# Performance work log

Measured on AMD Instinct MI355X. Metric: run time of the kernel, lower is better.

## Reference

```python
import jax, jax.numpy as jnp
import numpy as np

B, M, E, K, V, O = 2048, 131072, 256, 128, 256, 256
TOP_K = 3
THRESH = 0.0  # retrieval_threshold; default 0.5 but lowered so memory path is exercised
EPS = 1e-8


def setup_inputs() -> dict:
    key = jax.random.key(0)
    ks = jax.random.split(key, 20)
    w = lambda k, shape: jax.random.normal(k, shape, jnp.float32) * 0.02
    return {
        'state_embedding': jax.random.normal(ks[0], (B, E), jnp.float32),
        'keys': jax.random.normal(ks[1], (M, K), jnp.float32),
        'values': jax.random.normal(ks[2], (M, V), jnp.float32),
        'k_w1': w(ks[3], (E, 512)), 'k_b1': jnp.zeros((512,), jnp.float32),
        'k_w2': w(ks[4], (512, K)), 'k_b2': jnp.zeros((K,), jnp.float32),
        'a_w1': w(ks[5], (E + V, 128)), 'a_b1': jnp.zeros((128,), jnp.float32),
        'a_w2': w(ks[6], (128, 1)), 'a_b2': jnp.zeros((1,), jnp.float32),
        'i_w1': w(ks[7], (E + V, 512)), 'i_b1': jnp.zeros((512,), jnp.float32),
        'i_w2': w(ks[8], (512, O)), 'i_b2': jnp.zeros((O,), jnp.float32),
        'f_w1': w(ks[9], (E, 512)), 'f_b1': jnp.zeros((512,), jnp.float32),
        'f_w2': w(ks[10], (512, O)), 'f_b2': jnp.zeros((O,), jnp.float32),
    }


def _mann_forward(state_embedding, keys, values,
                  k_w1, k_b1, k_w2, k_b2,
                  a_w1, a_b1, a_w2, a_b2,
                  i_w1, i_b1, i_w2, i_b2,
                  f_w1, f_b1, f_w2, f_b2):
    # key_encoder: Linear -> ReLU -> Linear   [B, K]
    query = jax.nn.relu(state_embedding @ k_w1 + k_b1) @ k_w2 + k_b2
    # cosine similarity between query and the whole key bank  [B, M]
    qn = query / jnp.maximum(jnp.linalg.norm(query, axis=-1, keepdims=True), EPS)
    kn = keys / jnp.maximum(jnp.linalg.norm(keys, axis=-1, keepdims=True), EPS)
    sims = qn @ kn.T
    # iterative argmax+mask with threshold break == top-k then threshold mask
    top_vals, top_idx = jax.lax.top_k(sims, TOP_K)          # [B, TOP_K]
    hit = top_vals >= THRESH                                 # [B, TOP_K]
    retrieved = values[top_idx]                              # [B, TOP_K, V] gather
    # attention over retrieved memories conditioned on the state
    state_rep = jnp.broadcast_to(state_embedding[:, None, :], (state_embedding.shape[0], TOP_K, E))
    attn_in = jnp.concatenate([state_rep, retrieved], axis=-1)  # [B, TOP_K, E+V]
    h = jnp.tanh(attn_in @ a_w1 + a_b1)
    logits = (h @ a_w2 + a_b2)[..., 0]                       # [B, TOP_K]
    logits = jnp.where(hit, logits, -1e9)
    attn = jax.nn.softmax(logits, axis=-1)                   # [B, TOP_K]
    mem_vec = jnp.einsum('bk,bkv->bv', attn, retrieved)      # [B, V]
    # integration path (memory hit) vs fallback projection (miss)
    combined = jnp.concatenate([state_embedding, mem_vec], axis=-1)
    integrated = jax.nn.relu(combined @ i_w1 + i_b1) @ i_w2 + i_b2
    fallback = jax.nn.relu(state_embedding @ f_w1 + f_b1) @ f_w2 + f_b2
    any_hit = jnp.any(hit, axis=-1, keepdims=True)
    return jnp.where(any_hit, integrated, fallback)          # [B, O]


def reference(state_embedding, keys, values,
              k_w1, k_b1, k_w2, k_b2,
              a_w1, a_b1, a_w2, a_b2,
              i_w1, i_b1, i_w2, i_b2,
              f_w1, f_b1, f_w2, f_b2):
    return _mann_forward(state_embedding, keys, values,
                         k_w1, k_b1, k_w2, k_b2,
                         a_w1, a_b1, a_w2, a_b2,
                         i_w1, i_b1, i_w2, i_b2,
                         f_w1, f_b1, f_w2, f_b2)
```

## Files before the change

### kernel.cpp

```cpp
#include <hip/hip_runtime.h>
#include <math.h>

#define B_SZ 2048
#define M_SZ 131072
#define E_SZ 256
#define K_SZ 128
#define V_SZ 256
#define O_SZ 256

#define NCH  32
#define CH   (M_SZ / NCH)
#define BT   128
#define STG  64
#define NSTG (CH / STG)

#define WS_QN    0
#define WS_QNB   (WS_QN + B_SZ * K_SZ)
#define WS_KNB   (WS_QNB + B_SZ * K_SZ / 2)
#define WS_RNK   (WS_KNB + M_SZ * K_SZ / 2)
#define WS_CAND  (WS_RNK + M_SZ)
#define WS_TVAL  (WS_CAND + B_SZ * NCH * 16 * 3)
#define WS_TIDX  (WS_TVAL + B_SZ * 3)
#define WS_HENC  WS_CAND
#define WS_MEM   WS_CAND
#define WS_H2    (WS_CAND + B_SZ * V_SZ)
#define WS_HIT   (WS_H2 + B_SZ * 512)

#define NEG_INF (-3.0e38f)

typedef __attribute__((ext_vector_type(8))) short short8;
typedef __attribute__((ext_vector_type(4))) float f32x4;

static __device__ __forceinline__ void gl_lds16(const void* gptr, void* ldsptr) {
  __builtin_amdgcn_global_load_lds(
      (const __attribute__((address_space(1))) unsigned int*)gptr,
      (__attribute__((address_space(3))) unsigned int*)ldsptr, 16, 0, 0);
}

static __device__ __forceinline__ unsigned short f2bf(float x) {
  unsigned u = __float_as_uint(x);
  unsigned r = (u + 0x7FFFu + ((u >> 16) & 1u)) >> 16;
  return (unsigned short)r;
}
static __device__ __forceinline__ unsigned flipbf(unsigned short h) {
  return (h & 0x8000u) ? (unsigned)(h ^ 0xFFFFu) : (unsigned)(h | 0x8000u);
}

static __device__ __forceinline__ void ins3m(float (&tv)[3], float v, int kidx) {
  float vm = __uint_as_float((__float_as_uint(v) & 0xFFFFF000u) | (unsigned)kidx);
  float m0 = fmaxf(tv[0], vm), c0 = fminf(tv[0], vm);
  float m1 = fmaxf(tv[1], c0), c1 = fminf(tv[1], c0);
  float m2 = fmaxf(tv[2], c1);
  tv[0] = m0; tv[1] = m1; tv[2] = m2;
}
static __device__ __forceinline__ void ins3e(float (&tv)[3], float vm) {
  float m0 = fmaxf(tv[0], vm), c0 = fminf(tv[0], vm);
  float m1 = fmaxf(tv[1], c0), c1 = fminf(tv[1], c0);
  float m2 = fmaxf(tv[2], c1);
  tv[0] = m0; tv[1] = m1; tv[2] = m2;
}

static __device__ __forceinline__ void ins3u(unsigned (&tv)[3], int (&ti)[3], unsigned v, int m) {
  if (v > tv[2]) {
    if (v > tv[1]) {
      if (v > tv[0]) {
        tv[2] = tv[1]; ti[2] = ti[1]; tv[1] = tv[0]; ti[1] = ti[0]; tv[0] = v; ti[0] = m;
      } else {
        tv[2] = tv[1]; ti[2] = ti[1]; tv[1] = v; ti[1] = m;
      }
    } else {
      tv[2] = v; ti[2] = m;
    }
  }
}

__global__ __launch_bounds__(256)
void mann_enc1(const float* __restrict__ state,
               const float* __restrict__ k_w1,
               const float* __restrict__ k_b1,
               float* __restrict__ henc) {
  const int t = threadIdx.x;
  const int c = blockIdx.y * 256 + t;
  const int b0 = blockIdx.x * 4;
  float acc[4];
  const float bias = k_b1[c];
#pragma unroll
  for (int r = 0; r < 4; ++r) acc[r] = bias;
#pragma unroll 8
  for (int k = 0; k < 256; ++k) {
    const float w = k_w1[k * 512 + c];
#pragma unroll
    for (int r = 0; r < 4; ++r)
      acc[r] += state[(size_t)(b0 + r) * E_SZ + k] * w;
  }
#pragma unroll
  for (int r = 0; r < 4; ++r)
    henc[(size_t)(b0 + r) * 512 + c] = fmaxf(acc[r], 0.f);
}

__global__ __launch_bounds__(256)
void mann_enc2(const float* __restrict__ henc,
               const float* __restrict__ k_w2,
               const float* __restrict__ k_b2,
               float* __restrict__ qn,
               unsigned short* __restrict__ qnb) {
  __shared__ float s_red[4][128];
  __shared__ float s_part[2][4];
  const int t = threadIdx.x;
  const int col = t & 127, half = t >> 7;
  const int b0 = blockIdx.x * 4;
  float acc[4];
  const float bias = (half == 0) ? k_b2[col] : 0.f;
#pragma unroll
  for (int r = 0; r < 4; ++r) acc[r] = bias;
  const int kb = half * 256;
#pragma unroll 8
  for (int k = 0; k < 256; ++k) {
    const float wv = k_w2[(kb + k) * 128 + col];
#pragma unroll
    for (int r = 0; r < 4; ++r)
      acc[r] += henc[(size_t)(b0 + r) * 512 + kb + k] * wv;
  }
  if (half == 1)
#pragma unroll
    for (int r = 0; r < 4; ++r) s_red[r][col] = acc[r];
  __syncthreads();
  if (half == 0) {
#pragma unroll
    for (int r = 0; r < 4; ++r) acc[r] += s_red[r][col];
    const int l = t & 63, w = t >> 6;
    float ss[4];
#pragma unroll
    for (int r = 0; r < 4; ++r) ss[r] = acc[r] * acc[r];
#pragma unroll
    for (int off = 32; off > 0; off >>= 1)
#pragma unroll
      for (int r = 0; r < 4; ++r) ss[r] += __shfl_down(ss[r], off);
    if (l == 0)
#pragma unroll
      for (int r = 0; r < 4; ++r) s_part[w][r] = ss[r];
  }
  __syncthreads();
  if (half == 0) {
#pragma unroll
    for (int r = 0; r < 4; ++r) {
      float rn = 1.0f / fmaxf(sqrtf(s_part[0][r] + s_part[1][r]), 1e-8f);
      float q = acc[r] * rn;
      qn[(size_t)(b0 + r) * K_SZ + t] = q;
      qnb[(size_t)(b0 + r) * K_SZ + t] = f2bf(q);
    }
  }
}

__global__ void mann_keyprep(const float* __restrict__ keys,
                             unsigned short* __restrict__ knbsw,
                             float* __restrict__ rnk) {
  const int lane = threadIdx.x & 63;
  const int row = blockIdx.x * 4 + (threadIdx.x >> 6);
  const float* kr = keys + (size_t)row * K_SZ;
  float a = kr[lane], c = kr[lane + 64];
  float s = a * a + c * c;
#pragma unroll
  for (int off = 32; off > 0; off >>= 1) s += __shfl_down(s, off);
  float rn = 1.0f / fmaxf(sqrtf(__shfl(s, 0)), 1e-8f);
  if (lane == 0) rnk[row] = rn;
  const int r7 = row & 7;
  const int lp = lane & 31;
  const int src = ((((lp) >> 2) ^ r7) << 3) | ((2 * lp) & 7);
  float a0 = __shfl(a, src), a1 = __shfl(a, src + 1);
  float c0 = __shfl(c, src), c1 = __shfl(c, src + 1);
  float x0 = (lane < 32) ? a0 : c0;
  float x1 = (lane < 32) ? a1 : c1;
  unsigned pack = ((unsigned)f2bf(x1 * rn) << 16) | (unsigned)f2bf(x0 * rn);
  ((unsigned*)(knbsw + (size_t)row * 128))[lane] = pack;
}

__global__ __launch_bounds__(512, 4)
void mann_sims_mfma(const unsigned short* __restrict__ qnb,
                    const unsigned short* __restrict__ knbsw,
                    unsigned* __restrict__ cand) {
  __shared__ unsigned short s_k[2 * STG * 128];
  const int t = threadIdx.x;
  const int w = t >> 6, l = t & 63;
  const int wk = w >> 2;
  const int wr = w & 3;
  const int lo = l & 15, g = l >> 4;
  const int chunk = blockIdx.x, bt = blockIdx.y;
  const int b0 = bt * BT + wr * 32;
  const int k0 = chunk * CH;

  short8 afrag[2][4];
#pragma unroll
  for (int rti = 0; rti < 2; ++rti)
#pragma unroll
    for (int ks = 0; ks < 4; ++ks)
      afrag[rti][ks] = *(const short8*)(qnb + (size_t)(b0 + rti * 16 + lo) * K_SZ + ks * 32 + g * 8);

  float tv[2][4][3];
#pragma unroll
  for (int a = 0; a < 2; ++a)
#pragma unroll
    for (int b = 0; b < 4; ++b)
#pragma unroll
      for (int c = 0; c < 3; ++c) tv[a][b][c] = NEG_INF;

  const int ev = lo * 256 + ((g ^ (lo & 7)) << 4);
  const int od = ev ^ 64;
  const char* pev = (const char*)s_k + ev + wk * 8192;
  const char* pod = (const char*)s_k + od + wk * 8192;

  const char* gbase = (const char*)knbsw + (size_t)k0 * 256;
  char* lds0 = (char*)s_k;

#define ISSUE_STAGE(S, BUF)                                                  \
  do {                                                                       \
    const char* g0 = gbase + (size_t)(S) * 16384;                            \
    char* l0 = lds0 + (BUF) * 16384;                                         \
    _Pragma("unroll")                                                        \
    for (int i = 0; i < 2; ++i) {                                            \
      int seg = i * 8 + w;                                                   \
      gl_lds16(g0 + seg * 1024 + l * 16, l0 + seg * 1024);                   \
    }                                                                        \
  } while (0)

#define STAGE_CORE(S, BUF)                                                   \
  do {                                                                       \
    f32x4 cbuf[2][2];                                                        \
    __builtin_amdgcn_s_setprio(1);                                           \
    _Pragma("unroll")                                                        \
    for (int ktl = 0; ktl < 2; ++ktl) {                                      \
      short8 b0v = *(const short8*)(pev + (BUF) * 16384 + ktl * 4096);       \
      short8 b1v = *(const short8*)(pod + (BUF) * 16384 + ktl * 4096);       \
      short8 b2v = *(const short8*)(pev + (BUF) * 16384 + ktl * 4096 + 128); \
      short8 b3v = *(const short8*)(pod + (BUF) * 16384 + ktl * 4096 + 128); \
      _Pragma("unroll")                                                      \
      for (int rti = 0; rti < 2; ++rti) {                                    \
        f32x4 acc = {0.f, 0.f, 0.f, 0.f};                                    \
        acc = __builtin_amdgcn_mfma_f32_16x16x32_bf16(afrag[rti][0], b0v, acc, 0, 0, 0); \
        acc = __builtin_amdgcn_mfma_f32_16x16x32_bf16(afrag[rti][1], b1v, acc, 0, 0, 0); \
        acc = __builtin_amdgcn_mfma_f32_16x16x32_bf16(afrag[rti][2], b2v, acc, 0, 0, 0); \
        acc = __builtin_amdgcn_mfma_f32_16x16x32_bf16(afrag[rti][3], b3v, acc, 0, 0, 0); \
        cbuf[rti][ktl] = acc;                                                \
      }                                                                      \
    }                                                                        \
    __builtin_amdgcn_s_setprio(0);                                           \
    _Pragma("unroll")                                                        \
    for (int ktl = 0; ktl < 2; ++ktl) {                                      \
      const int kidx = (S) * STG + (wk * 2 + ktl) * 16 + lo;                 \
      _Pragma("unroll")                                                      \
      for (int rti = 0; rti < 2; ++rti) {                                    \
        ins3m(tv[rti][0], cbuf[rti][ktl][0], kidx);                          \
        ins3m(tv[rti][1], cbuf[rti][ktl][1], kidx);                          \
        ins3m(tv[rti][2], cbuf[rti][ktl][2], kidx);                          \
        ins3m(tv[rti][3], cbuf[rti][ktl][3], kidx);                          \
      }                                                                      \
    }                                                                        \
  } while (0)

  ISSUE_STAGE(0, 0);

  for (int s = 0; s < NSTG; s += 2) {
    __syncthreads();
    if (s + 1 < NSTG) ISSUE_STAGE(s + 1, 1);
    STAGE_CORE(s, 0);
    __syncthreads();
    if (s + 2 < NSTG) ISSUE_STAGE(s + 2, 0);
    STAGE_CORE(s + 1, 1);
  }
#undef STAGE_CORE
#undef ISSUE_STAGE

  __syncthreads();
  unsigned* lm = (unsigned*)s_k;
  if (wk == 1) {
#pragma unroll
    for (int rti = 0; rti < 2; ++rti)
#pragma unroll
      for (int j = 0; j < 4; ++j)
#pragma unroll
        for (int slot = 0; slot < 3; ++slot)
          lm[((wr * 64 + l) * 2 + rti) * 12 + j * 3 + slot] =
              __float_as_uint(tv[rti][j][slot]);
  }
  __syncthreads();
  if (wk == 0) {
#pragma unroll
    for (int rti = 0; rti < 2; ++rti)
#pragma unroll
      for (int j = 0; j < 4; ++j)
#pragma unroll
        for (int slot = 0; slot < 3; ++slot) {
          float bv = __uint_as_float(lm[((wr * 64 + l) * 2 + rti) * 12 + j * 3 + slot]);
          ins3e(tv[rti][j], bv);
        }
#pragma unroll
    for (int rti = 0; rti < 2; ++rti) {
#pragma unroll
      for (int j = 0; j < 4; ++j) {
        int b = b0 + rti * 16 + g * 4 + j;
        size_t base = (((size_t)b * NCH + chunk) * 16 + lo) * 3;
#pragma unroll
        for (int slot = 0; slot < 3; ++slot) {
          unsigned bits = __float_as_uint(tv[rti][j][slot]);
          float val = __uint_as_float(bits & 0xFFFFF000u);
          unsigned idx = bits & 0xFFFu;
          unsigned p = (flipbf(f2bf(val)) << 16) | idx;
          cand[base + slot] = p;
        }
      }
    }
  }
}

__global__ void mann_merge_rescore(const unsigned* __restrict__ cand,
                                   const float* __restrict__ qn,
                                   const float* __restrict__ keys,
                                   const float* __restrict__ rnk,
                                   float* __restrict__ tval,
                                   int* __restrict__ tidx) {
  __shared__ unsigned s_pv[4][192];
  __shared__ int s_gi[4][192];
  __shared__ float s_ex[4][8];
  const int t = threadIdx.x;
  const int w = t >> 6, l = t & 63;
  const int b = blockIdx.x * 4 + w;
  const int NCAND = NCH * 16 * 3;

  unsigned pv[3] = {0u, 0u, 0u};
  int gi[3] = {0, 0, 0};
  for (int k = 0; k < NCAND / 64; ++k) {
    int i = l + k * 64;
    unsigned p = cand[(size_t)b * NCAND + i];
    int gidx = (i / 48) * CH + (int)(p & 0xFFFu);
    ins3u(pv, gi, p, gidx);
  }
#pragma unroll
  for (int j = 0; j < 3; ++j) { s_pv[w][l * 3 + j] = pv[j]; s_gi[w][l * 3 + j] = gi[j]; }
  __syncthreads();

  if (l == 0) {
    unsigned bv[8]; int bg[8];
#pragma unroll
    for (int j = 0; j < 8; ++j) { bv[j] = 0u; bg[j] = 0; }
    for (int i = 0; i < 192; ++i) {
      unsigned p = s_pv[w][i];
      if (p > bv[7]) {
        int gg = s_gi[w][i];
        int j = 7;
        while (j > 0 && p > bv[j - 1]) { bv[j] = bv[j - 1]; bg[j] = bg[j - 1]; --j; }
        bv[j] = p; bg[j] = gg;
      }
    }
#pragma unroll
    for (int j = 0; j < 8; ++j) s_gi[w][j] = bg[j];
  }
  __syncthreads();

  float q0 = qn[(size_t)b * K_SZ + l];
  float q1 = qn[(size_t)b * K_SZ + 64 + l];
#pragma unroll
  for (int d = 0; d < 8; ++d) {
    int idx = s_gi[w][d];
    float p = q0 * keys[(size_t)idx * K_SZ + l] + q1 * keys[(size_t)idx * K_SZ + 64 + l];
#pragma unroll
    for (int off = 32; off > 0; off >>= 1) p += __shfl_down(p, off);
    if (l == 0) s_ex[w][d] = p * rnk[idx];
  }
  __syncthreads();

  if (l == 0) {
    unsigned used = 0;
#pragma unroll
    for (int r = 0; r < 3; ++r) {
      float best = NEG_INF; int bd = 0;
      for (int d = 0; d < 8; ++d)
        if (!(used & (1u << d)) && s_ex[w][d] > best) { best = s_ex[w][d]; bd = d; }
      used |= (1u << bd);
      tval[b * 3 + r] = best;
      tidx[b * 3 + r] = s_gi[w][bd];
    }
  }
}

__global__ __launch_bounds__(128)
void mann_t1(const float* __restrict__ state,
             const float* __restrict__ values,
             const float* __restrict__ tval,
             const int* __restrict__ tidx,
             const float* __restrict__ a_w1, const float* __restrict__ a_b1,
             const float* __restrict__ a_w2, const float* __restrict__ a_b2,
             float* __restrict__ mem, int* __restrict__ hit) {
  __shared__ float s_h1[6][128];
  __shared__ float s_logit[6];
  __shared__ float s_attn[2][3];
  const int t = threadIdx.x;
  const int b0 = blockIdx.x * 2;

  float racc[2];
  {
    const float bias = a_b1[t];
#pragma unroll
    for (int r = 0; r < 2; ++r) racc[r] = bias;
  }
#pragma unroll 4
  for (int k = 0; k < 256; ++k) {
    const float w = a_w1[k * 128 + t];
#pragma unroll
    for (int r = 0; r < 2; ++r)
      racc[r] += state[(size_t)(b0 + r) * E_SZ + k] * w;
  }
  float pacc[6];
#pragma unroll
  for (int p = 0; p < 6; ++p) pacc[p] = racc[p / 3];
#pragma unroll 4
  for (int k = 0; k < 256; ++k) {
    const float w = a_w1[(256 + k) * 128 + t];
#pragma unroll
    for (int p = 0; p < 6; ++p) {
      const int vrow = tidx[(b0 + p / 3) * 3 + (p % 3)];
      pacc[p] += values[(size_t)vrow * V_SZ + k] * w;
    }
  }
#pragma unroll
  for (int p = 0; p < 6; ++p) s_h1[p][t] = tanhf(pacc[p]);
  __syncthreads();

  if (t < 48) {
    const int p = t >> 3, l8 = t & 7;
    float acc = 0.f;
    for (int i = l8; i < 128; i += 8)
      acc += s_h1[p][i] * a_w2[i];
#pragma unroll
    for (int off = 4; off > 0; off >>= 1) acc += __shfl_down(acc, off, 8);
    if (l8 == 0) s_logit[p] = acc + a_b2[0];
  }
  __syncthreads();

  if (t < 2) {
    const int b = b0 + t;
    bool h0 = tval[b * 3 + 0] >= 0.0f;
    bool h1 = tval[b * 3 + 1] >= 0.0f;
    bool h2 = tval[b * 3 + 2] >= 0.0f;
    float l0 = h0 ? s_logit[t * 3 + 0] : -1e9f;
    float l1 = h1 ? s_logit[t * 3 + 1] : -1e9f;
    float l2 = h2 ? s_logit[t * 3 + 2] : -1e9f;
    float mx = fmaxf(l0, fmaxf(l1, l2));
    float e0 = expf(l0 - mx), e1 = expf(l1 - mx), e2 = expf(l2 - mx);
    float inv = 1.0f / (e0 + e1 + e2);
    s_attn[t][0] = e0 * inv; s_attn[t][1] = e1 * inv; s_attn[t][2] = e2 * inv;
    hit[b] = (h0 || h1 || h2) ? 1 : 0;
  }
  __syncthreads();

#pragma unroll
  for (int r = 0; r < 2; ++r) {
    const int i0 = tidx[(b0 + r) * 3 + 0];
    const int i1 = tidx[(b0 + r) * 3 + 1];
    const int i2 = tidx[(b0 + r) * 3 + 2];
    const float a0 = s_attn[r][0], a1 = s_attn[r][1], a2 = s_attn[r][2];
#pragma unroll
    for (int h = 0; h < 2; ++h) {
      const int c = t + h * 128;
      mem[(size_t)(b0 + r) * V_SZ + c] =
          a0 * values[(size_t)i0 * V_SZ + c] +
          a1 * values[(size_t)i1 * V_SZ + c] +
          a2 * values[(size_t)i2 * V_SZ + c];
    }
  }
}

__global__ __launch_bounds__(256)
void mann_t2a(const float* __restrict__ state,
              const float* __restrict__ mem,
              const float* __restrict__ i_w1, const float* __restrict__ i_b1,
              float* __restrict__ h2) {
  const int t = threadIdx.x;
  const int c = blockIdx.y * 256 + t;
  const int b0 = blockIdx.x * 4;
  float acc[4];
  const float bias = i_b1[c];
#pragma unroll
  for (int r = 0; r < 4; ++r) acc[r] = bias;
#pragma unroll 8
  for (int k = 0; k < 256; ++k) {
    const float w = i_w1[k * 512 + c];
#pragma unroll
    for (int r = 0; r < 4; ++r)
      acc[r] += state[(size_t)(b0 + r) * E_SZ + k] * w;
  }
#pragma unroll 8
  for (int k = 0; k < 256; ++k) {
    const float w = i_w1[(256 + k) * 512 + c];
#pragma unroll
    for (int r = 0; r < 4; ++r)
      acc[r] += mem[(size_t)(b0 + r) * V_SZ + k] * w;
  }
#pragma unroll
  for (int r = 0; r < 4; ++r)
    h2[(size_t)(b0 + r) * 512 + c] = fmaxf(acc[r], 0.f);
}

__global__ __launch_bounds__(256)
void mann_t2b(const float* __restrict__ h2,
              const float* __restrict__ state,
              const int* __restrict__ hit,
              const float* __restrict__ i_w2, const float* __restrict__ i_b2,
              const float* __restrict__ f_w1, const float* __restrict__ f_b1,
              const float* __restrict__ f_w2, const float* __restrict__ f_b2,
              float* __restrict__ out) {
  __shared__ float s_fh[512];
  const int t = threadIdx.x;
  const int b0 = blockIdx.x * 2;
  float acc[2];
  const float bias = i_b2[t];
#pragma unroll
  for (int r = 0; r < 2; ++r) acc[r] = bias;
#pragma unroll 8
  for (int k = 0; k < 512; ++k) {
    const float w = i_w2[k * 256 + t];
#pragma unroll
    for (int r = 0; r < 2; ++r)
      acc[r] += h2[(size_t)(b0 + r) * 512 + k] * w;
  }
#pragma unroll
  for (int r = 0; r < 2; ++r) {
    if (hit[b0 + r]) {
      out[(size_t)(b0 + r) * O_SZ + t] = acc[r];
    } else {
      __syncthreads();
#pragma unroll
      for (int h = 0; h < 2; ++h) {
        const int j = t + h * 256;
        float a = f_b1[j];
        for (int k = 0; k < 256; ++k)
          a += state[(size_t)(b0 + r) * E_SZ + k] * f_w1[k * 512 + j];
        s_fh[j] = fmaxf(a, 0.f);
      }
      __syncthreads();
      float o = f_b2[t];
      for (int k = 0; k < 512; ++k) o += s_fh[k] * f_w2[k * 256 + t];
      out[(size_t)(b0 + r) * O_SZ + t] = o;
    }
  }
}

extern "C" void kernel_launch(void* const* d_in, const int* in_sizes, int n_in,
                              void* d_out, int out_size, void* d_ws, size_t ws_size,
                              hipStream_t stream) {
  const float* state = (const float*)d_in[0];
  const float* keys  = (const float*)d_in[1];
  const float* values = (const float*)d_in[2];
  const float* k_w1 = (const float*)d_in[3];
  const float* k_b1 = (const float*)d_in[4];
  const float* k_w2 = (const float*)d_in[5];
  const float* k_b2 = (const float*)d_in[6];
  const float* a_w1 = (const float*)d_in[7];
  const float* a_b1 = (const float*)d_in[8];
  const float* a_w2 = (const float*)d_in[9];
  const float* a_b2 = (const float*)d_in[10];
  const float* i_w1 = (const float*)d_in[11];
  const float* i_b1 = (const float*)d_in[12];
  const float* i_w2 = (const float*)d_in[13];
  const float* i_b2 = (const float*)d_in[14];
  const float* f_w1 = (const float*)d_in[15];
  const float* f_b1 = (const float*)d_in[16];
  const float* f_w2 = (const float*)d_in[17];
  const float* f_b2 = (const float*)d_in[18];
  float* out = (float*)d_out;

  float* ws = (float*)d_ws;
  float* qn = ws + WS_QN;
  unsigned short* qnb = (unsigned short*)(ws + WS_QNB);
  unsigned short* knbsw = (unsigned short*)(ws + WS_KNB);
  float* rnk = ws + WS_RNK;
  unsigned* cand = (unsigned*)(ws + WS_CAND);
  float* tvalp = ws + WS_TVAL;
  int* tidxp = (int*)(ws + WS_TIDX);
  float* henc = ws + WS_HENC;
  float* memv = ws + WS_MEM;
  float* h2 = ws + WS_H2;
  int* hitp = (int*)(ws + WS_HIT);

  mann_enc1<<<dim3(B_SZ / 4, 2), 256, 0, stream>>>(state, k_w1, k_b1, henc);
  mann_enc2<<<B_SZ / 4, 256, 0, stream>>>(henc, k_w2, k_b2, qn, qnb);
  mann_keyprep<<<M_SZ / 4, 256, 0, stream>>>(keys, knbsw, rnk);
  mann_sims_mfma<<<dim3(NCH, B_SZ / BT), 512, 0, stream>>>(qnb, knbsw, cand);
  mann_merge_rescore<<<B_SZ / 4, 256, 0, stream>>>(cand, qn, keys, rnk, tvalp, tidxp);
  mann_t1<<<B_SZ / 2, 128, 0, stream>>>(state, values, tvalp, tidxp,
                                        a_w1, a_b1, a_w2, a_b2, memv, hitp);
  mann_t2a<<<dim3(B_SZ / 4, 2), 256, 0, stream>>>(state, memv, i_w1, i_b1, h2);
  mann_t2b<<<B_SZ / 2, 256, 0, stream>>>(h2, state, hitp, i_w2, i_b2,
                                         f_w1, f_b1, f_w2, f_b2, out);
}
```

Baseline: 556.8 us.

## Swap MFMA operand roles and stream keys directly from pre-fragmented global layout

Key prep now writes normalized bf16 keys in MFMA A-fragment order in 16-row groups, so the sims kernel can read them from global memory straight into registers without LDS staging. The query tile now sits in LDS and registers as the B operand. Each wave scans its own slice of keys and keeps a per-lane top-3, which removes the cross-wave LDS merge and the double-buffer syncs. The trade-off is that key reads now depend on direct global latency with only one tile of prefetch, and the query tile per block drops from 128 to 64 rows, so key-bank traffic doubles.

```diff
diff --git a/kernel.cpp b/kernel.cpp
--- a/kernel.cpp
+++ b/kernel.cpp
@@ -10,9 +10,6 @@
 
 #define NCH  32
 #define CH   (M_SZ / NCH)
-#define BT   128
-#define STG  64
-#define NSTG (CH / STG)
 
 #define WS_QN    0
 #define WS_QNB   (WS_QN + B_SZ * K_SZ)
@@ -30,6 +27,7 @@
 
 typedef __attribute__((ext_vector_type(8))) short short8;
 typedef __attribute__((ext_vector_type(4))) float f32x4;
+typedef __attribute__((ext_vector_type(4))) unsigned uint4v;
 
 static __device__ __forceinline__ void gl_lds16(const void* gptr, void* ldsptr) {
   __builtin_amdgcn_global_load_lds(
@@ -48,12 +46,6 @@
 
 static __device__ __forceinline__ void ins3m(float (&tv)[3], float v, int kidx) {
   float vm = __uint_as_float((__float_as_uint(v) & 0xFFFFF000u) | (unsigned)kidx);
-  float m0 = fmaxf(tv[0], vm), c0 = fminf(tv[0], vm);
-  float m1 = fmaxf(tv[1], c0), c1 = fminf(tv[1], c0);
-  float m2 = fmaxf(tv[2], c1);
-  tv[0] = m0; tv[1] = m1; tv[2] = m2;
-}
-static __device__ __forceinline__ void ins3e(float (&tv)[3], float vm) {
   float m0 = fmaxf(tv[0], vm), c0 = fminf(tv[0], vm);
   float m1 = fmaxf(tv[1], c0), c1 = fminf(tv[1], c0);
   float m2 = fmaxf(tv[2], c1);
@@ -152,162 +144,125 @@
   }
 }
 
-__global__ void mann_keyprep(const float* __restrict__ keys,
-                             unsigned short* __restrict__ knbsw,
-                             float* __restrict__ rnk) {
-  const int lane = threadIdx.x & 63;
-  const int row = blockIdx.x * 4 + (threadIdx.x >> 6);
-  const float* kr = keys + (size_t)row * K_SZ;
-  float a = kr[lane], c = kr[lane + 64];
-  float s = a * a + c * c;
-#pragma unroll
-  for (int off = 32; off > 0; off >>= 1) s += __shfl_down(s, off);
-  float rn = 1.0f / fmaxf(sqrtf(__shfl(s, 0)), 1e-8f);
-  if (lane == 0) rnk[row] = rn;
-  const int r7 = row & 7;
-  const int lp = lane & 31;
-  const int src = ((((lp) >> 2) ^ r7) << 3) | ((2 * lp) & 7);
-  float a0 = __shfl(a, src), a1 = __shfl(a, src + 1);
-  float c0 = __shfl(c, src), c1 = __shfl(c, src + 1);
-  float x0 = (lane < 32) ? a0 : c0;
-  float x1 = (lane < 32) ? a1 : c1;
-  unsigned pack = ((unsigned)f2bf(x1 * rn) << 16) | (unsigned)f2bf(x0 * rn);
-  ((unsigned*)(knbsw + (size_t)row * 128))[lane] = pack;
-}
-
-__global__ __launch_bounds__(512, 4)
+__global__ __launch_bounds__(256)
+void mann_keyprep(const float* __restrict__ keys,
+                  unsigned short* __restrict__ knbA,
+                  float* __restrict__ rnk) {
+  __shared__ float s_k[16][132];
+  __shared__ float s_pp[16][16];
+  const int t = threadIdx.x;
+  const int kg = blockIdx.x;
+  const float* gk = keys + (size_t)kg * (16 * 128);
+#pragma unroll
+  for (int i = 0; i < 8; ++i) {
+    int idx = t + i * 256;
+    s_k[idx >> 7][idx & 127] = gk[idx];
+  }
+  __syncthreads();
+  const int row = t & 15, sl = t >> 4;
+  float p = 0.f;
+#pragma unroll
+  for (int e = 0; e < 8; ++e) {
+    float x = s_k[row][sl + 16 * e];
+    p += x * x;
+  }
+  s_pp[row][sl] = p;
+  __syncthreads();
+  float s = 0.f;
+#pragma unroll
+  for (int x = 0; x < 16; ++x) s += s_pp[row][x];
+  float rn = 1.0f / fmaxf(sqrtf(s), 1e-8f);
+  if (t < 16) rnk[kg * 16 + t] = rn;
+  const int wg = (t >> 4) & 3, ks = t >> 6;
+  unsigned pk[4];
+#pragma unroll
+  for (int h = 0; h < 4; ++h) {
+    float x0 = s_k[row][ks * 32 + wg * 8 + 2 * h] * rn;
+    float x1 = s_k[row][ks * 32 + wg * 8 + 2 * h + 1] * rn;
+    pk[h] = ((unsigned)f2bf(x1) << 16) | (unsigned)f2bf(x0);
+  }
+  uint4v v; v.x = pk[0]; v.y = pk[1]; v.z = pk[2]; v.w = pk[3];
+  *(uint4v*)((char*)knbA + (size_t)kg * 4096 + t * 16) = v;
+}
+
+__global__ __launch_bounds__(256, 4)
 void mann_sims_mfma(const unsigned short* __restrict__ qnb,
-                    const unsigned short* __restrict__ knbsw,
+                    const unsigned short* __restrict__ knbA,
                     unsigned* __restrict__ cand) {
-  __shared__ unsigned short s_k[2 * STG * 128];
-  const int t = threadIdx.x;
-  const int w = t >> 6, l = t & 63;
-  const int wk = w >> 2;
-  const int wr = w & 3;
+  __shared__ unsigned short s_q[64 * 128];
+  const int t = threadIdx.x;
+  const int wv = t >> 6, l = t & 63;
   const int lo = l & 15, g = l >> 4;
   const int chunk = blockIdx.x, bt = blockIdx.y;
-  const int b0 = bt * BT + wr * 32;
-  const int k0 = chunk * CH;
-
-  short8 afrag[2][4];
-#pragma unroll
-  for (int rti = 0; rti < 2; ++rti)
+  const int b0 = bt * 64;
+
+  {
+    const char* gq = (const char*)qnb + (size_t)b0 * 256;
+    char* lq = (char*)s_q;
+#pragma unroll
+    for (int i = 0; i < 4; ++i)
+      gl_lds16(gq + i * 4096 + wv * 1024 + l * 16, lq + i * 4096 + wv * 1024 + l * 16);
+  }
+  __syncthreads();
+
+  short8 bf[4][4];
+#pragma unroll
+  for (int rg = 0; rg < 4; ++rg)
 #pragma unroll
     for (int ks = 0; ks < 4; ++ks)
-      afrag[rti][ks] = *(const short8*)(qnb + (size_t)(b0 + rti * 16 + lo) * K_SZ + ks * 32 + g * 8);
-
-  float tv[2][4][3];
-#pragma unroll
-  for (int a = 0; a < 2; ++a)
-#pragma unroll
-    for (int b = 0; b < 4; ++b)
-#pragma unroll
-      for (int c = 0; c < 3; ++c) tv[a][b][c] = NEG_INF;
-
-  const int ev = lo * 256 + ((g ^ (lo & 7)) << 4);
-  const int od = ev ^ 64;
-  const char* pev = (const char*)s_k + ev + wk * 8192;
-  const char* pod = (const char*)s_k + od + wk * 8192;
-
-  const char* gbase = (const char*)knbsw + (size_t)k0 * 256;
-  char* lds0 = (char*)s_k;
-
-#define ISSUE_STAGE(S, BUF)                                                  \
-  do {                                                                       \
-    const char* g0 = gbase + (size_t)(S) * 16384;                            \
-    char* l0 = lds0 + (BUF) * 16384;                                         \
-    _Pragma("unroll")                                                        \
-    for (int i = 0; i < 2; ++i) {                                            \
-      int seg = i * 8 + w;                                                   \
-      gl_lds16(g0 + seg * 1024 + l * 16, l0 + seg * 1024);                   \
-    }                                                                        \
-  } while (0)
-
-#define STAGE_CORE(S, BUF)                                                   \
-  do {                                                                       \
-    f32x4 cbuf[2][2];                                                        \
-    __builtin_amdgcn_s_setprio(1);                                           \
-    _Pragma("unroll")                                                        \
-    for (int ktl = 0; ktl < 2; ++ktl) {                                      \
-      short8 b0v = *(const short8*)(pev + (BUF) * 16384 + ktl * 4096);       \
-      short8 b1v = *(const short8*)(pod + (BUF) * 16384 + ktl * 4096);       \
-      short8 b2v = *(const short8*)(pev + (BUF) * 16384 + ktl * 4096 + 128); \
-      short8 b3v = *(const short8*)(pod + (BUF) * 16384 + ktl * 4096 + 128); \
-      _Pragma("unroll")                                                      \
-      for (int rti = 0; rti < 2; ++rti) {                                    \
-        f32x4 acc = {0.f, 0.f, 0.f, 0.f};                                    \
-        acc = __builtin_amdgcn_mfma_f32_16x16x32_bf16(afrag[rti][0], b0v, acc, 0, 0, 0); \
-        acc = __builtin_amdgcn_mfma_f32_16x16x32_bf16(afrag[rti][1], b1v, acc, 0, 0, 0); \
-        acc = __builtin_amdgcn_mfma_f32_16x16x32_bf16(afrag[rti][2], b2v, acc, 0, 0, 0); \
-        acc = __builtin_amdgcn_mfma_f32_16x16x32_bf16(afrag[rti][3], b3v, acc, 0, 0, 0); \
-        cbuf[rti][ktl] = acc;                                                \
-      }                                                                      \
-    }                                                                        \
-    __builtin_amdgcn_s_setprio(0);                                           \
-    _Pragma("unroll")                                                        \
-    for (int ktl = 0; ktl < 2; ++ktl) {                                      \
-      const int kidx = (S) * STG + (wk * 2 + ktl) * 16 + lo;                 \
-      _Pragma("unroll")                                                      \
-      for (int rti = 0; rti < 2; ++rti) {                                    \
-        ins3m(tv[rti][0], cbuf[rti][ktl][0], kidx);                          \
-        ins3m(tv[rti][1], cbuf[rti][ktl][1], kidx);                          \
-        ins3m(tv[rti][2], cbuf[rti][ktl][2], kidx);                          \
-        ins3m(tv[rti][3], cbuf[rti][ktl][3], kidx);                          \
-      }                                                                      \
-    }                                                                        \
-  } while (0)
-
-  ISSUE_STAGE(0, 0);
-
-  for (int s = 0; s < NSTG; s += 2) {
-    __syncthreads();
-    if (s + 1 < NSTG) ISSUE_STAGE(s + 1, 1);
-    STAGE_CORE(s, 0);
-    __syncthreads();
-    if (s + 2 < NSTG) ISSUE_STAGE(s + 2, 0);
-    STAGE_CORE(s + 1, 1);
-  }
-#undef STAGE_CORE
-#undef ISSUE_STAGE
-
-  __syncthreads();
-  unsigned* lm = (unsigned*)s_k;
-  if (wk == 1) {
-#pragma unroll
-    for (int rti = 0; rti < 2; ++rti)
-#pragma unroll
-      for (int j = 0; j < 4; ++j)
-#pragma unroll
-        for (int slot = 0; slot < 3; ++slot)
-          lm[((wr * 64 + l) * 2 + rti) * 12 + j * 3 + slot] =
-              __float_as_uint(tv[rti][j][slot]);
-  }
-  __syncthreads();
-  if (wk == 0) {
-#pragma unroll
-    for (int rti = 0; rti < 2; ++rti)
-#pragma unroll
-      for (int j = 0; j < 4; ++j)
-#pragma unroll
-        for (int slot = 0; slot < 3; ++slot) {
-          float bv = __uint_as_float(lm[((wr * 64 + l) * 2 + rti) * 12 + j * 3 + slot]);
-          ins3e(tv[rti][j], bv);
-        }
-#pragma unroll
-    for (int rti = 0; rti < 2; ++rti) {
-#pragma unroll
-      for (int j = 0; j < 4; ++j) {
-        int b = b0 + rti * 16 + g * 4 + j;
-        size_t base = (((size_t)b * NCH + chunk) * 16 + lo) * 3;
-#pragma unroll
-        for (int slot = 0; slot < 3; ++slot) {
-          unsigned bits = __float_as_uint(tv[rti][j][slot]);
-          float val = __uint_as_float(bits & 0xFFFFF000u);
-          unsigned idx = bits & 0xFFFu;
-          unsigned p = (flipbf(f2bf(val)) << 16) | idx;
-          cand[base + slot] = p;
-        }
-      }
+      bf[rg][ks] = *(const short8*)((const char*)s_q + (rg * 16 + lo) * 256 + ks * 64 + g * 16);
+
+  float tv[4][3];
+#pragma unroll
+  for (int rg = 0; rg < 4; ++rg)
+#pragma unroll
+    for (int c = 0; c < 3; ++c) tv[rg][c] = NEG_INF;
+
+  const char* kp = (const char*)knbA + ((size_t)chunk * (CH / 16) + wv * 64) * 4096;
+
+  short8 af[4];
+#pragma unroll
+  for (int ks = 0; ks < 4; ++ks)
+    af[ks] = *(const short8*)(kp + ks * 1024 + l * 16);
+
+  for (int it = 0; it < 64; ++it) {
+    f32x4 a0 = {0.f, 0.f, 0.f, 0.f};
+    f32x4 a1 = {0.f, 0.f, 0.f, 0.f};
+    f32x4 a2 = {0.f, 0.f, 0.f, 0.f};
+    f32x4 a3 = {0.f, 0.f, 0.f, 0.f};
+#pragma unroll
+    for (int ks = 0; ks < 4; ++ks) {
+      a0 = __builtin_amdgcn_mfma_f32_16x16x32_bf16(af[ks], bf[0][ks], a0, 0, 0, 0);
+      a1 = __builtin_amdgcn_mfma_f32_16x16x32_bf16(af[ks], bf[1][ks], a1, 0, 0, 0);
+      a2 = __builtin_amdgcn_mfma_f32_16x16x32_bf16(af[ks], bf[2][ks], a2, 0, 0, 0);
+      a3 = __builtin_amdgcn_mfma_f32_16x16x32_bf16(af[ks], bf[3][ks], a3, 0, 0, 0);
+    }
+    if (it + 1 < 64) {
+      kp += 4096;
+#pragma unroll
+      for (int ks = 0; ks < 4; ++ks)
+        af[ks] = *(const short8*)(kp + ks * 1024 + l * 16);
+    }
+    const int kb = wv * 1024 + it * 16 + g * 4;
+#pragma unroll
+    for (int j = 0; j < 4; ++j) {
+      ins3m(tv[0], a0[j], kb + j);
+      ins3m(tv[1], a1[j], kb + j);
+      ins3m(tv[2], a2[j], kb + j);
+      ins3m(tv[3], a3[j], kb + j);
+    }
+  }
+
+#pragma unroll
+  for (int rg = 0; rg < 4; ++rg) {
+    const int b = b0 + rg * 16 + lo;
+    size_t base = (((size_t)b * NCH + chunk) * 16 + (wv * 4 + g)) * 3;
+#pragma unroll
+    for (int slot = 0; slot < 3; ++slot) {
+      unsigned bits = __float_as_uint(tv[rg][slot]);
+      float val = __uint_as_float(bits & 0xFFFFF000u);
+      unsigned p = (flipbf(f2bf(val)) << 16) | (bits & 0xFFFu);
+      cand[base + slot] = p;
     }
   }
 }
@@ -571,7 +526,7 @@
   float* ws = (float*)d_ws;
   float* qn = ws + WS_QN;
   unsigned short* qnb = (unsigned short*)(ws + WS_QNB);
-  unsigned short* knbsw = (unsigned short*)(ws + WS_KNB);
+  unsigned short* knbA = (unsigned short*)(ws + WS_KNB);
   float* rnk = ws + WS_RNK;
   unsigned* cand = (unsigned*)(ws + WS_CAND);
   float* tvalp = ws + WS_TVAL;
@@ -583,8 +538,8 @@
 
   mann_enc1<<<dim3(B_SZ / 4, 2), 256, 0, stream>>>(state, k_w1, k_b1, henc);
   mann_enc2<<<B_SZ / 4, 256, 0, stream>>>(henc, k_w2, k_b2, qn, qnb);
-  mann_keyprep<<<M_SZ / 4, 256, 0, stream>>>(keys, knbsw, rnk);
-  mann_sims_mfma<<<dim3(NCH, B_SZ / BT), 512, 0, stream>>>(qnb, knbsw, cand);
+  mann_keyprep<<<M_SZ / 16, 256, 0, stream>>>(keys, knbA, rnk);
+  mann_sims_mfma<<<dim3(NCH, B_SZ / 64), 256, 0, stream>>>(qnb, knbA, cand);
   mann_merge_rescore<<<B_SZ / 4, 256, 0, stream>>>(cand, qn, keys, rnk, tvalp, tidxp);
   mann_t1<<<B_SZ / 2, 128, 0, stream>>>(state, values, tvalp, tidxp,
                                         a_w1, a_b1, a_w2, a_b2, memv, hitp);
```

Result: faster. 540.6 us (-2.9%).
